# Kernel tuning notes

Hardware: AMD Instinct MI355X
Metric: run time of the kernel (lower is better)

The kernel has to match this reference:

```python
import jax, jax.numpy as jnp
import numpy as np

EMBED_DIM = 1280
NUM_HEADS = 20
HEAD_DIM = EMBED_DIM // NUM_HEADS


def setup_inputs() -> dict:
    key = jax.random.key(0)
    ks = jax.random.split(key, 9)
    s = 0.02
    return {
        "hidden_states": jax.random.normal(ks[0], (4, 1500, EMBED_DIM), dtype=jnp.float32),
        "q_w": jax.random.normal(ks[1], (EMBED_DIM, EMBED_DIM), dtype=jnp.float32) * s,
        "q_b": jax.random.normal(ks[2], (EMBED_DIM,), dtype=jnp.float32) * s,
        "k_w": jax.random.normal(ks[3], (EMBED_DIM, EMBED_DIM), dtype=jnp.float32) * s,
        "v_w": jax.random.normal(ks[4], (EMBED_DIM, EMBED_DIM), dtype=jnp.float32) * s,
        "v_b": jax.random.normal(ks[5], (EMBED_DIM,), dtype=jnp.float32) * s,
        "o_w": jax.random.normal(ks[6], (EMBED_DIM, EMBED_DIM), dtype=jnp.float32) * s,
        "o_b": jax.random.normal(ks[7], (EMBED_DIM,), dtype=jnp.float32) * s,
    }


def reference(hidden_states, q_w, q_b, k_w, v_w, v_b, o_w, o_b):
    B, T, E = hidden_states.shape
    H, D = NUM_HEADS, HEAD_DIM
    scaling = D ** (-0.5)
    # projections (torch Linear: x @ W^T + b)
    q = (hidden_states @ q_w.T + q_b) * scaling
    k = hidden_states @ k_w.T  # k_proj has bias=False
    v = hidden_states @ v_w.T + v_b
    # [B, H, T, D]
    q = q.reshape(B, T, H, D).transpose(0, 2, 1, 3)
    k = k.reshape(B, T, H, D).transpose(0, 2, 1, 3)
    v = v.reshape(B, T, H, D).transpose(0, 2, 1, 3)
    # NOTE: module divides by sqrt(head_dim) AGAIN inside the kernel (faithful)
    scores = jnp.einsum("bhqd,bhkd->bhqk", q, k) / jnp.sqrt(jnp.asarray(D, q.dtype))
    attn = jax.nn.softmax(scores, axis=-1)
    out = jnp.einsum("bhqk,bhkd->bhqd", attn, v)
    out = out.transpose(0, 2, 1, 3).reshape(B, T, E)
    return out @ o_w.T + o_b
```

## Files before the change

### kernel.cpp

```cpp
#include <hip/hip_runtime.h>

typedef __attribute__((ext_vector_type(4))) float f32x4;
typedef __attribute__((ext_vector_type(8))) __bf16 bf16x8;
typedef __attribute__((ext_vector_type(4))) __bf16 bf16x4;

#define DEV __device__ __forceinline__

DEV f32x4 mfma_bf16(bf16x8 a, bf16x8 b, f32x4 c) {
  return __builtin_amdgcn_mfma_f32_16x16x32_bf16(a, b, c, 0, 0, 0);
}

DEV void glds16(const void* gp, void* lp) {
  __builtin_amdgcn_global_load_lds((const __attribute__((address_space(1))) void*)gp,
                                   (__attribute__((address_space(3))) void*)lp, 16, 0, 0);
}

DEV float fast_exp2(float x) {
#if __has_builtin(__builtin_amdgcn_exp2f)
  return __builtin_amdgcn_exp2f(x);
#else
  float r;
  asm("v_exp_f32 %0, %1" : "=v"(r) : "v"(x));
  return r;
#endif
}

#define SB0() __builtin_amdgcn_sched_barrier(0)

__global__ __launch_bounds__(256) void cvt_bf16(const float* __restrict__ in,
                                                __bf16* __restrict__ out, int n_in) {
  long long i = (long long)blockIdx.x * 256 + threadIdx.x;
  long long e = i * 8;
  bf16x8 o = {};
  if (e < n_in) {
    const f32x4* ip = (const f32x4*)(in + e);
    f32x4 a = ip[0], b = ip[1];
#pragma unroll
    for (int j = 0; j < 4; ++j) { o[j] = (__bf16)a[j]; o[j + 4] = (__bf16)b[j]; }
  }
  *(bf16x8*)(out + e) = o;
}

__global__ __launch_bounds__(256) void cvt_w4(const float* __restrict__ a, const float* __restrict__ b,
                                              const float* __restrict__ c, const float* __restrict__ d,
                                              __bf16* __restrict__ oa, __bf16* __restrict__ ob,
                                              __bf16* __restrict__ oc, __bf16* __restrict__ od) {
  int blk = blockIdx.x;
  int which = blk / 800;
  int bb = blk - which * 800;
  const float* in = which == 0 ? a : which == 1 ? b : which == 2 ? c : d;
  __bf16* out = which == 0 ? oa : which == 1 ? ob : which == 2 ? oc : od;
  long long e = ((long long)bb * 256 + threadIdx.x) * 8;
  const f32x4* ip = (const f32x4*)(in + e);
  f32x4 x = ip[0], y = ip[1];
  bf16x8 o;
#pragma unroll
  for (int j = 0; j < 4; ++j) { o[j] = (__bf16)x[j]; o[j + 4] = (__bf16)y[j]; }
  *(bf16x8*)(out + e) = o;
}

__global__ __launch_bounds__(512, 2) void gemm_qkv(const __bf16* __restrict__ A,
                                                   const __bf16* __restrict__ Bw,
                                                   const float* __restrict__ qbias,
                                                   const float* __restrict__ vbias,
                                                   __bf16* __restrict__ Qo,
                                                   __bf16* __restrict__ Ko,
                                                   __bf16* __restrict__ Vto,
                                                   float sq) {
  __shared__ __align__(16) __bf16 lds[3 * 24576];
  const int tid = threadIdx.x;
  const int lane = tid & 63, wave = tid >> 6;
  const int wrow = wave >> 2, wcol = wave & 3;
  const int r = lane & 15, g = lane >> 4;

  const int orig = blockIdx.x;
  const int xcd = orig & 7, ii = orig >> 3;
  const int m_idx = xcd * 6 + ii % 6;
  const int n_idx = ii / 6;
  const int m0 = m_idx * 128, n0 = n_idx * 256;

  const f32x4 fz = {0.f, 0.f, 0.f, 0.f};
  f32x4 acc[4][4];
#pragma unroll
  for (int mi = 0; mi < 4; ++mi)
#pragma unroll
    for (int ni = 0; ni < 4; ++ni) acc[mi][ni] = fz;

  const __bf16* srcA[2];
  const __bf16* srcB[4];
#pragma unroll
  for (int j = 0; j < 2; ++j) {
    const int slot = j * 512 + tid;
    const int row = slot >> 3, ch = slot & 7;
    srcA[j] = A + (size_t)(m0 + row) * 1280 + (ch ^ (row & 7)) * 8;
  }
#pragma unroll
  for (int j = 0; j < 4; ++j) {
    const int slot = j * 512 + tid;
    const int row = slot >> 3, ch = slot & 7;
    srcB[j] = Bw + (size_t)(n0 + row) * 1280 + (ch ^ (row & 7)) * 8;
  }
  const int wdst = wave * 512;

  auto stage_h0 = [&](int buf, int kt2) {
    const int k0 = kt2 * 64;
    glds16(srcA[0] + k0, &lds[buf * 24576 + wdst]);
    glds16(srcA[1] + k0, &lds[buf * 24576 + 4096 + wdst]);
    glds16(srcB[0] + k0, &lds[buf * 24576 + 8192 + wdst]);
  };
  auto stage_h1 = [&](int buf, int kt2) {
    const int k0 = kt2 * 64;
    glds16(srcB[1] + k0, &lds[buf * 24576 + 12288 + wdst]);
    glds16(srcB[2] + k0, &lds[buf * 24576 + 16384 + wdst]);
    glds16(srcB[3] + k0, &lds[buf * 24576 + 20480 + wdst]);
  };

  stage_h0(0, 0); stage_h1(0, 0);
  stage_h0(1, 1); stage_h1(1, 1);
  asm volatile("s_waitcnt vmcnt(6)" ::: "memory");
  SB0();
  __builtin_amdgcn_s_barrier();
  SB0();

  const int aoff = (wrow * 64 + r) * 64;
  const int boff = 8192 + (wcol * 64 + r) * 64;
  const int c0 = (g ^ (r & 7)) * 8;
  const int c1 = ((4 + g) ^ (r & 7)) * 8;

  int cur = 0;
  for (int kt = 0; kt < 20; ++kt) {
    int nxt2 = cur + 2; if (nxt2 >= 3) nxt2 -= 3;
    const __bf16* Lb = &lds[cur * 24576];
    const bool pf = (kt + 2 < 20);

    bf16x8 af[4], bfr[4];
#pragma unroll
    for (int mi = 0; mi < 4; ++mi) af[mi] = *(const bf16x8*)&Lb[aoff + mi * 1024 + c0];
#pragma unroll
    for (int ni = 0; ni < 4; ++ni) bfr[ni] = *(const bf16x8*)&Lb[boff + ni * 1024 + c0];
    if (pf) stage_h0(nxt2, kt + 2);
    asm volatile("s_waitcnt lgkmcnt(0)" ::: "memory");
    SB0();
    __builtin_amdgcn_s_setprio(1);
#pragma unroll
    for (int mi = 0; mi < 4; ++mi)
#pragma unroll
      for (int ni = 0; ni < 4; ++ni)
        acc[mi][ni] = mfma_bf16(af[mi], bfr[ni], acc[mi][ni]);
    __builtin_amdgcn_s_setprio(0);

    bf16x8 af1[4], bfr1[4];
#pragma unroll
    for (int mi = 0; mi < 4; ++mi) af1[mi] = *(const bf16x8*)&Lb[aoff + mi * 1024 + c1];
#pragma unroll
    for (int ni = 0; ni < 4; ++ni) bfr1[ni] = *(const bf16x8*)&Lb[boff + ni * 1024 + c1];
    if (pf) stage_h1(nxt2, kt + 2);
    asm volatile("s_waitcnt lgkmcnt(0)" ::: "memory");
    SB0();
    __builtin_amdgcn_s_setprio(1);
#pragma unroll
    for (int mi = 0; mi < 4; ++mi)
#pragma unroll
      for (int ni = 0; ni < 4; ++ni)
        acc[mi][ni] = mfma_bf16(af1[mi], bfr1[ni], acc[mi][ni]);
    __builtin_amdgcn_s_setprio(0);

    if (pf) asm volatile("s_waitcnt vmcnt(6)" ::: "memory");
    else    asm volatile("s_waitcnt vmcnt(0)" ::: "memory");
    SB0();
    __builtin_amdgcn_s_barrier();
    SB0();
    cur = cur + 1; if (cur >= 3) cur -= 3;
  }

  const int which = n_idx / 5;
  const int nb = n0 - which * 1280 + wcol * 64;
  const float scale = (which == 0) ? sq : 1.f;

#pragma unroll
  for (int ni = 0; ni < 4; ++ni) {
    const int col = nb + ni * 16 + r;
    const float bv = (which == 0) ? qbias[col] : (which == 2) ? vbias[col] : 0.f;
#pragma unroll
    for (int mi = 0; mi < 4; ++mi) {
      if (which == 2) {
        const int row0 = m0 + wrow * 64 + mi * 16 + g * 4;
        if (row0 < 6000) {
          const int bidx = row0 / 1500;
          const int t = row0 - bidx * 1500;
          union { __bf16 h[4]; unsigned long long u; } pk;
#pragma unroll
          for (int rr = 0; rr < 4; ++rr) pk.h[rr] = (__bf16)(acc[mi][ni][rr] + bv);
          *(unsigned long long*)&Vto[((size_t)(bidx * 1280 + col)) * 1536 + t] = pk.u;
        }
      } else {
        __bf16* dst = (which == 0) ? Qo : Ko;
#pragma unroll
        for (int rr = 0; rr < 4; ++rr) {
          const int row = m0 + wrow * 64 + mi * 16 + g * 4 + rr;
          dst[(size_t)row * 1280 + col] = (__bf16)((acc[mi][ni][rr] + bv) * scale);
        }
      }
    }
  }
}

__global__ __launch_bounds__(256) void gemm_o(const __bf16* __restrict__ A,
                                              const __bf16* __restrict__ Bw,
                                              const float* __restrict__ bias,
                                              float* __restrict__ out) {
  __shared__ __align__(16) __bf16 lds[2 * 8192];
  const int tid = threadIdx.x;
  const int lane = tid & 63, wave = tid >> 6;
  const int orig = blockIdx.x;
  const int xcd = orig & 7, i = orig >> 3;
  const int m_idx = (xcd & 3) * 12 + i % 12;
  const int n_idx = (xcd >> 2) * 5 + i / 12;
  const int m0 = m_idx * 128, n0 = n_idx * 128;
  const int wm = (wave >> 1) * 64, wn = (wave & 1) * 64;
  const int r = lane & 15, g = lane >> 4;

  const f32x4 fz = {0.f, 0.f, 0.f, 0.f};
  f32x4 acc[4][4];
#pragma unroll
  for (int mi = 0; mi < 4; ++mi)
#pragma unroll
    for (int ni = 0; ni < 4; ++ni) acc[mi][ni] = fz;

  const int cg = 8 * ((tid & 3) ^ ((tid >> 3) & 3));
  const __bf16* Abase = A + (size_t)(m0 + (tid >> 2)) * 1280 + cg;
  const __bf16* Bbase = Bw + (size_t)(n0 + (tid >> 2)) * 1280 + cg;
  const int wA = wave * 512;
  const int csw = (g ^ ((lane >> 1) & 3)) * 8;

  auto stage = [&](int buf, int kt2) {
    const int k0 = kt2 * 32;
    __bf16* L = &lds[buf * 8192];
    glds16(Abase + k0, L + wA);
    glds16(Abase + 64 * 1280 + k0, L + wA + 2048);
    glds16(Bbase + k0, L + 4096 + wA);
    glds16(Bbase + 64 * 1280 + k0, L + 6144 + wA);
  };

  stage(0, 0);
  for (int kt = 0; kt < 40; ++kt) {
    const int cur = kt & 1;
    if (kt + 1 < 40) {
      stage(cur ^ 1, kt + 1);
      asm volatile("s_waitcnt vmcnt(4)" ::: "memory");
    } else {
      asm volatile("s_waitcnt vmcnt(0)" ::: "memory");
    }
    SB0();
    __builtin_amdgcn_s_barrier();
    SB0();

    const __bf16* Ab = &lds[cur * 8192];
    const __bf16* Bb = Ab + 4096;
    bf16x8 af[4], bfr[4];
#pragma unroll
    for (int mi = 0; mi < 4; ++mi)
      af[mi] = *(const bf16x8*)&Ab[(wm + mi * 16 + r) * 32 + csw];
#pragma unroll
    for (int ni = 0; ni < 4; ++ni)
      bfr[ni] = *(const bf16x8*)&Bb[(wn + ni * 16 + r) * 32 + csw];
#pragma unroll
    for (int mi = 0; mi < 4; ++mi)
#pragma unroll
      for (int ni = 0; ni < 4; ++ni)
        acc[mi][ni] = mfma_bf16(af[mi], bfr[ni], acc[mi][ni]);

    asm volatile("s_waitcnt lgkmcnt(0)" ::: "memory");
    SB0();
    __builtin_amdgcn_s_barrier();
    SB0();
  }

#pragma unroll
  for (int ni = 0; ni < 4; ++ni) {
    const int col = n0 + wn + ni * 16 + r;
    const float bv = bias[col];
#pragma unroll
    for (int mi = 0; mi < 4; ++mi) {
#pragma unroll
      for (int rr = 0; rr < 4; ++rr) {
        const int row = m0 + wm + mi * 16 + g * 4 + rr;
        if (row < 6000) out[(size_t)row * 1280 + col] = acc[mi][ni][rr] + bv;
      }
    }
  }
}

__global__ __launch_bounds__(256) void flash_attn(const __bf16* __restrict__ Qg,
                                                  const __bf16* __restrict__ Kg,
                                                  const __bf16* __restrict__ Vt,
                                                  __bf16* __restrict__ Og) {
  constexpr int TQ = 1500, NKT = 24;
  __shared__ __align__(16) __bf16 lds[16384];

  const int tid = threadIdx.x;
  const int lane = tid & 63, w = tid >> 6;
  const int r = lane & 15, g = lane >> 4;

  const int orig = blockIdx.x;
  const int work = (orig & 7) * 120 + (orig >> 3);
  const int bh = work / 12, qb = work - bh * 12;
  const int b = bh / 20, h = bh - b * 20;
  const int q0 = qb * 128;
  const size_t base = (size_t)b * (TQ * 1280) + h * 64;
  const __bf16* Vt_bh = Vt + (size_t)(b * 1280 + h * 64) * 1536;

  const int k_src_col = 8 * ((lane & 7) ^ (lane >> 3));
  const int k_row_loc = w * 8 + (lane >> 3);
  const int v_d_loc = 8 * w + (lane >> 3);
  const int v_chunk = 8 * ((lane & 7) ^ (lane >> 3));

  bf16x8 qf[2][2];
#pragma unroll
  for (int qs = 0; qs < 2; ++qs) {
    int t = q0 + w * 32 + qs * 16 + r;
    t = t < TQ ? t : TQ - 1;
    const __bf16* qp = Qg + base + (size_t)t * 1280;
#pragma unroll
    for (int dk = 0; dk < 2; ++dk) qf[qs][dk] = *(const bf16x8*)(qp + dk * 32 + g * 8);
  }

  const f32x4 fz = {0.f, 0.f, 0.f, 0.f};
  f32x4 o_acc[2][4];
#pragma unroll
  for (int qs = 0; qs < 2; ++qs)
#pragma unroll
    for (int ni = 0; ni < 4; ++ni) o_acc[qs][ni] = fz;
  float l_run[2] = {0.f, 0.f};

  auto stage = [&](int buf, int kt2) {
    const int kb = kt2 * 64;
#pragma unroll
    for (int i = 0; i < 2; ++i) {
      int row = kb + i * 32 + k_row_loc;
      row = row < TQ ? row : TQ - 1;
      glds16(Kg + base + (size_t)row * 1280 + k_src_col,
             &lds[buf * 8192 + i * 2048 + w * 512]);
    }
#pragma unroll
    for (int i = 0; i < 2; ++i) {
      glds16(Vt_bh + (size_t)(32 * i + v_d_loc) * 1536 + kb + v_chunk,
             &lds[buf * 8192 + 4096 + i * 2048 + w * 512]);
    }
  };

  stage(0, 0);
  __syncthreads();
  for (int kt = 0; kt < NKT; ++kt) {
    const int cur = kt & 1;
    if (kt + 1 < NKT) stage(cur ^ 1, kt + 1);

    const __bf16* Kb = &lds[cur * 8192];

    f32x4 s[2][4];
#pragma unroll
    for (int qs = 0; qs < 2; ++qs)
#pragma unroll
      for (int nt = 0; nt < 4; ++nt) s[qs][nt] = fz;
#pragma unroll
    for (int dk = 0; dk < 2; ++dk) {
      bf16x8 kf[4];
#pragma unroll
      for (int nt = 0; nt < 4; ++nt) {
        const int row = nt * 16 + r;
        const int sc = (dk * 32 + g * 8) ^ ((r & 7) << 3);
        kf[nt] = *(const bf16x8*)&Kb[row * 64 + sc];
      }
#pragma unroll
      for (int qs = 0; qs < 2; ++qs)
#pragma unroll
        for (int nt = 0; nt < 4; ++nt) s[qs][nt] = mfma_bf16(kf[nt], qf[qs][dk], s[qs][nt]);
    }

    if (kt == NKT - 1) {
#pragma unroll
      for (int nt = 0; nt < 4; ++nt)
#pragma unroll
        for (int rr = 0; rr < 4; ++rr) {
          const int key = kt * 64 + nt * 16 + g * 4 + rr;
          if (key >= TQ) { s[0][nt][rr] = -1.0e30f; s[1][nt][rr] = -1.0e30f; }
        }
    }

#pragma unroll
    for (int qs = 0; qs < 2; ++qs) {
      float ssum = 0.f;
#pragma unroll
      for (int nt = 0; nt < 4; ++nt)
#pragma unroll
        for (int rr = 0; rr < 4; ++rr) {
          const float p = fast_exp2(s[qs][nt][rr]);
          s[qs][nt][rr] = p;
          ssum += p;
        }
      l_run[qs] += ssum;
    }

    const __bf16* Vbuf = &lds[cur * 8192 + 4096];
    const int swz = (r & 7) << 3;
#pragma unroll
    for (int ks = 0; ks < 2; ++ks) {
      bf16x8 pa[2];
#pragma unroll
      for (int qs = 0; qs < 2; ++qs) {
        bf16x8 t;
#pragma unroll
        for (int j = 0; j < 4; ++j) {
          t[j] = (__bf16)s[qs][2 * ks][j];
          t[4 + j] = (__bf16)s[qs][2 * ks + 1][j];
        }
        pa[qs] = t;
      }
      const int o1 = (32 * ks + 4 * g) ^ swz;
      const int o2 = (32 * ks + 16 + 4 * g) ^ swz;
#pragma unroll
      for (int ni = 0; ni < 4; ++ni) {
        const int dbase = (16 * ni + r) * 64;
        union { bf16x4 hh[2]; bf16x8 v; } u;
        u.hh[0] = *(const bf16x4*)&Vbuf[dbase + o1];
        u.hh[1] = *(const bf16x4*)&Vbuf[dbase + o2];
#pragma unroll
        for (int qs = 0; qs < 2; ++qs) o_acc[qs][ni] = mfma_bf16(u.v, pa[qs], o_acc[qs][ni]);
      }
    }

    __syncthreads();
  }

  float inv[2];
#pragma unroll
  for (int qs = 0; qs < 2; ++qs) {
    float l = l_run[qs];
    l += __shfl_xor(l, 16);
    l += __shfl_xor(l, 32);
    inv[qs] = 1.0f / l;
  }

  __bf16* Ob = &lds[w * 2304];
#pragma unroll
  for (int qs = 0; qs < 2; ++qs) {
#pragma unroll
    for (int ni = 0; ni < 4; ++ni)
#pragma unroll
      for (int rr = 0; rr < 4; ++rr)
        Ob[(qs * 16 + r) * 72 + ni * 16 + g * 4 + rr] = (__bf16)(o_acc[qs][ni][rr] * inv[qs]);
  }
  __syncthreads();
  const int qg = q0 + w * 32 + (lane >> 1);
  if (qg < TQ) {
#pragma unroll
    for (int v = 0; v < 4; ++v) {
      const int c = (lane & 1) * 32 + v * 8;
      bf16x8 val = *(const bf16x8*)&lds[w * 2304 + (lane >> 1) * 72 + c];
      *(bf16x8*)&Og[base + (size_t)qg * 1280 + c] = val;
    }
  }
}

extern "C" void kernel_launch(void* const* d_in, const int* in_sizes, int n_in,
                              void* d_out, int out_size, void* d_ws, size_t ws_size,
                              hipStream_t stream) {
  const float* hs = (const float*)d_in[0];
  const float* qw = (const float*)d_in[1];
  const float* qb = (const float*)d_in[2];
  const float* kw = (const float*)d_in[3];
  const float* vw = (const float*)d_in[4];
  const float* vb = (const float*)d_in[5];
  const float* ow = (const float*)d_in[6];
  const float* ob = (const float*)d_in[7];

  const long long MP = 6144LL * 1280;
  const long long WE = 1280LL * 1280;
  __bf16* Xb = (__bf16*)d_ws;
  __bf16* Wq = Xb + MP;
  __bf16* Wk = Wq + WE;
  __bf16* Wv = Wk + WE;
  __bf16* Wo = Wv + WE;
  __bf16* Qb = Wo + WE;
  __bf16* Kb = Qb + MP;
  __bf16* Vtb = Kb + MP;
  __bf16* Ab = Xb;

  cvt_bf16<<<3840, 256, 0, stream>>>(hs, Xb, 7680000);
  cvt_w4<<<3200, 256, 0, stream>>>(qw, kw, vw, ow, Wq, Wk, Wv, Wo);

  const float SQ = 1.4426950408889634f / 64.f;
  gemm_qkv<<<720, 512, 0, stream>>>(Xb, Wq, qb, vb, Qb, Kb, Vtb, SQ);

  flash_attn<<<960, 256, 0, stream>>>(Qb, Kb, Vtb, Ab);

  gemm_o<<<480, 256, 0, stream>>>(Ab, Wo, ob, (float*)d_out);
}
```

Baseline: 180.2 us.

## Merge conversion kernels, retile output GEMM with triple buffering, tighten attention sync

Fuses the activation and weight fp32-to-bf16 conversion kernels into one launch to save a launch. Rewrites the output projection GEMM to use 512-thread blocks with 128x256 tiles, K-step 64, a three-stage LDS pipeline with split prefetch and s_setprio around the MFMA blocks. Replaces the __syncthreads in flash attention with explicit vmcnt/lgkmcnt waits plus raw barriers, so the next tile's prefetch is waited on before its use. The larger GEMM tiles leave only 240 blocks, which may underfill the device's compute units.

```diff
diff --git a/kernel.cpp b/kernel.cpp
--- a/kernel.cpp
+++ b/kernel.cpp
@@ -27,36 +27,41 @@
 
 #define SB0() __builtin_amdgcn_sched_barrier(0)
 
-__global__ __launch_bounds__(256) void cvt_bf16(const float* __restrict__ in,
-                                                __bf16* __restrict__ out, int n_in) {
-  long long i = (long long)blockIdx.x * 256 + threadIdx.x;
-  long long e = i * 8;
-  bf16x8 o = {};
-  if (e < n_in) {
+__global__ __launch_bounds__(256) void cvt_all(const float* __restrict__ hs,
+                                               const float* __restrict__ qw,
+                                               const float* __restrict__ kw,
+                                               const float* __restrict__ vw,
+                                               const float* __restrict__ ow,
+                                               __bf16* __restrict__ oX,
+                                               __bf16* __restrict__ oQ,
+                                               __bf16* __restrict__ oK,
+                                               __bf16* __restrict__ oV,
+                                               __bf16* __restrict__ oO) {
+  const int blk = blockIdx.x;
+  if (blk < 3840) {
+    long long e = ((long long)blk * 256 + threadIdx.x) * 8;
+    bf16x8 o = {};
+    if (e < 7680000) {
+      const f32x4* ip = (const f32x4*)(hs + e);
+      f32x4 a = ip[0], b = ip[1];
+#pragma unroll
+      for (int j = 0; j < 4; ++j) { o[j] = (__bf16)a[j]; o[j + 4] = (__bf16)b[j]; }
+    }
+    *(bf16x8*)(oX + e) = o;
+  } else {
+    const int wb = blk - 3840;
+    const int which = wb / 800;
+    const int bb = wb - which * 800;
+    const float* in = which == 0 ? qw : which == 1 ? kw : which == 2 ? vw : ow;
+    __bf16* out = which == 0 ? oQ : which == 1 ? oK : which == 2 ? oV : oO;
+    long long e = ((long long)bb * 256 + threadIdx.x) * 8;
     const f32x4* ip = (const f32x4*)(in + e);
-    f32x4 a = ip[0], b = ip[1];
-#pragma unroll
-    for (int j = 0; j < 4; ++j) { o[j] = (__bf16)a[j]; o[j + 4] = (__bf16)b[j]; }
-  }
-  *(bf16x8*)(out + e) = o;
-}
-
-__global__ __launch_bounds__(256) void cvt_w4(const float* __restrict__ a, const float* __restrict__ b,
-                                              const float* __restrict__ c, const float* __restrict__ d,
-                                              __bf16* __restrict__ oa, __bf16* __restrict__ ob,
-                                              __bf16* __restrict__ oc, __bf16* __restrict__ od) {
-  int blk = blockIdx.x;
-  int which = blk / 800;
-  int bb = blk - which * 800;
-  const float* in = which == 0 ? a : which == 1 ? b : which == 2 ? c : d;
-  __bf16* out = which == 0 ? oa : which == 1 ? ob : which == 2 ? oc : od;
-  long long e = ((long long)bb * 256 + threadIdx.x) * 8;
-  const f32x4* ip = (const f32x4*)(in + e);
-  f32x4 x = ip[0], y = ip[1];
-  bf16x8 o;
-#pragma unroll
-  for (int j = 0; j < 4; ++j) { o[j] = (__bf16)x[j]; o[j + 4] = (__bf16)y[j]; }
-  *(bf16x8*)(out + e) = o;
+    f32x4 x = ip[0], y = ip[1];
+    bf16x8 o;
+#pragma unroll
+    for (int j = 0; j < 4; ++j) { o[j] = (__bf16)x[j]; o[j + 4] = (__bf16)y[j]; }
+    *(bf16x8*)(out + e) = o;
+  }
 }
 
 __global__ __launch_bounds__(512, 2) void gemm_qkv(const __bf16* __restrict__ A,
@@ -205,20 +210,21 @@
   }
 }
 
-__global__ __launch_bounds__(256) void gemm_o(const __bf16* __restrict__ A,
-                                              const __bf16* __restrict__ Bw,
-                                              const float* __restrict__ bias,
-                                              float* __restrict__ out) {
-  __shared__ __align__(16) __bf16 lds[2 * 8192];
+__global__ __launch_bounds__(512, 2) void gemm_o(const __bf16* __restrict__ A,
+                                                 const __bf16* __restrict__ Bw,
+                                                 const float* __restrict__ bias,
+                                                 float* __restrict__ out) {
+  __shared__ __align__(16) __bf16 lds[3 * 24576];
   const int tid = threadIdx.x;
   const int lane = tid & 63, wave = tid >> 6;
+  const int wrow = wave >> 2, wcol = wave & 3;
+  const int r = lane & 15, g = lane >> 4;
+
   const int orig = blockIdx.x;
-  const int xcd = orig & 7, i = orig >> 3;
-  const int m_idx = (xcd & 3) * 12 + i % 12;
-  const int n_idx = (xcd >> 2) * 5 + i / 12;
-  const int m0 = m_idx * 128, n0 = n_idx * 128;
-  const int wm = (wave >> 1) * 64, wn = (wave & 1) * 64;
-  const int r = lane & 15, g = lane >> 4;
+  const int xcd = orig & 7, ii = orig >> 3;
+  const int m_idx = xcd * 6 + ii % 6;
+  const int n_idx = ii / 6;
+  const int m0 = m_idx * 128, n0 = n_idx * 256;
 
   const f32x4 fz = {0.f, 0.f, 0.f, 0.f};
   f32x4 acc[4][4];
@@ -227,64 +233,102 @@
 #pragma unroll
     for (int ni = 0; ni < 4; ++ni) acc[mi][ni] = fz;
 
-  const int cg = 8 * ((tid & 3) ^ ((tid >> 3) & 3));
-  const __bf16* Abase = A + (size_t)(m0 + (tid >> 2)) * 1280 + cg;
-  const __bf16* Bbase = Bw + (size_t)(n0 + (tid >> 2)) * 1280 + cg;
-  const int wA = wave * 512;
-  const int csw = (g ^ ((lane >> 1) & 3)) * 8;
-
-  auto stage = [&](int buf, int kt2) {
-    const int k0 = kt2 * 32;
-    __bf16* L = &lds[buf * 8192];
-    glds16(Abase + k0, L + wA);
-    glds16(Abase + 64 * 1280 + k0, L + wA + 2048);
-    glds16(Bbase + k0, L + 4096 + wA);
-    glds16(Bbase + 64 * 1280 + k0, L + 6144 + wA);
+  const __bf16* srcA[2];
+  const __bf16* srcB[4];
+#pragma unroll
+  for (int j = 0; j < 2; ++j) {
+    const int slot = j * 512 + tid;
+    const int row = slot >> 3, ch = slot & 7;
+    srcA[j] = A + (size_t)(m0 + row) * 1280 + (ch ^ (row & 7)) * 8;
+  }
+#pragma unroll
+  for (int j = 0; j < 4; ++j) {
+    const int slot = j * 512 + tid;
+    const int row = slot >> 3, ch = slot & 7;
+    srcB[j] = Bw + (size_t)(n0 + row) * 1280 + (ch ^ (row & 7)) * 8;
+  }
+  const int wdst = wave * 512;
+
+  auto stage_h0 = [&](int buf, int kt2) {
+    const int k0 = kt2 * 64;
+    glds16(srcA[0] + k0, &lds[buf * 24576 + wdst]);
+    glds16(srcA[1] + k0, &lds[buf * 24576 + 4096 + wdst]);
+    glds16(srcB[0] + k0, &lds[buf * 24576 + 8192 + wdst]);
   };
-
-  stage(0, 0);
-  for (int kt = 0; kt < 40; ++kt) {
-    const int cur = kt & 1;
-    if (kt + 1 < 40) {
-      stage(cur ^ 1, kt + 1);
-      asm volatile("s_waitcnt vmcnt(4)" ::: "memory");
-    } else {
-      asm volatile("s_waitcnt vmcnt(0)" ::: "memory");
-    }
-    SB0();
-    __builtin_amdgcn_s_barrier();
-    SB0();
-
-    const __bf16* Ab = &lds[cur * 8192];
-    const __bf16* Bb = Ab + 4096;
+  auto stage_h1 = [&](int buf, int kt2) {
+    const int k0 = kt2 * 64;
+    glds16(srcB[1] + k0, &lds[buf * 24576 + 12288 + wdst]);
+    glds16(srcB[2] + k0, &lds[buf * 24576 + 16384 + wdst]);
+    glds16(srcB[3] + k0, &lds[buf * 24576 + 20480 + wdst]);
+  };
+
+  stage_h0(0, 0); stage_h1(0, 0);
+  stage_h0(1, 1); stage_h1(1, 1);
+  asm volatile("s_waitcnt vmcnt(6)" ::: "memory");
+  SB0();
+  __builtin_amdgcn_s_barrier();
+  SB0();
+
+  const int aoff = (wrow * 64 + r) * 64;
+  const int boff = 8192 + (wcol * 64 + r) * 64;
+  const int c0 = (g ^ (r & 7)) * 8;
+  const int c1 = ((4 + g) ^ (r & 7)) * 8;
+
+  int cur = 0;
+  for (int kt = 0; kt < 20; ++kt) {
+    int nxt2 = cur + 2; if (nxt2 >= 3) nxt2 -= 3;
+    const __bf16* Lb = &lds[cur * 24576];
+    const bool pf = (kt + 2 < 20);
+
     bf16x8 af[4], bfr[4];
 #pragma unroll
-    for (int mi = 0; mi < 4; ++mi)
-      af[mi] = *(const bf16x8*)&Ab[(wm + mi * 16 + r) * 32 + csw];
-#pragma unroll
-    for (int ni = 0; ni < 4; ++ni)
-      bfr[ni] = *(const bf16x8*)&Bb[(wn + ni * 16 + r) * 32 + csw];
+    for (int mi = 0; mi < 4; ++mi) af[mi] = *(const bf16x8*)&Lb[aoff + mi * 1024 + c0];
+#pragma unroll
+    for (int ni = 0; ni < 4; ++ni) bfr[ni] = *(const bf16x8*)&Lb[boff + ni * 1024 + c0];
+    if (pf) stage_h0(nxt2, kt + 2);
+    asm volatile("s_waitcnt lgkmcnt(0)" ::: "memory");
+    SB0();
+    __builtin_amdgcn_s_setprio(1);
 #pragma unroll
     for (int mi = 0; mi < 4; ++mi)
 #pragma unroll
       for (int ni = 0; ni < 4; ++ni)
         acc[mi][ni] = mfma_bf16(af[mi], bfr[ni], acc[mi][ni]);
-
+    __builtin_amdgcn_s_setprio(0);
+
+    bf16x8 af1[4], bfr1[4];
+#pragma unroll
+    for (int mi = 0; mi < 4; ++mi) af1[mi] = *(const bf16x8*)&Lb[aoff + mi * 1024 + c1];
+#pragma unroll
+    for (int ni = 0; ni < 4; ++ni) bfr1[ni] = *(const bf16x8*)&Lb[boff + ni * 1024 + c1];
+    if (pf) stage_h1(nxt2, kt + 2);
     asm volatile("s_waitcnt lgkmcnt(0)" ::: "memory");
     SB0();
+    __builtin_amdgcn_s_setprio(1);
+#pragma unroll
+    for (int mi = 0; mi < 4; ++mi)
+#pragma unroll
+      for (int ni = 0; ni < 4; ++ni)
+        acc[mi][ni] = mfma_bf16(af1[mi], bfr1[ni], acc[mi][ni]);
+    __builtin_amdgcn_s_setprio(0);
+
+    if (pf) asm volatile("s_waitcnt vmcnt(6)" ::: "memory");
+    else    asm volatile("s_waitcnt vmcnt(0)" ::: "memory");
+    SB0();
     __builtin_amdgcn_s_barrier();
     SB0();
+    cur = cur + 1; if (cur >= 3) cur -= 3;
   }
 
 #pragma unroll
   for (int ni = 0; ni < 4; ++ni) {
-    const int col = n0 + wn + ni * 16 + r;
+    const int col = n0 + wcol * 64 + ni * 16 + r;
     const float bv = bias[col];
 #pragma unroll
     for (int mi = 0; mi < 4; ++mi) {
 #pragma unroll
       for (int rr = 0; rr < 4; ++rr) {
-        const int row = m0 + wm + mi * 16 + g * 4 + rr;
+        const int row = m0 + wrow * 64 + mi * 16 + g * 4 + rr;
         if (row < 6000) out[(size_t)row * 1280 + col] = acc[mi][ni][rr] + bv;
       }
     }
@@ -350,10 +394,17 @@
   };
 
   stage(0, 0);
-  __syncthreads();
   for (int kt = 0; kt < NKT; ++kt) {
     const int cur = kt & 1;
-    if (kt + 1 < NKT) stage(cur ^ 1, kt + 1);
+    if (kt + 1 < NKT) {
+      stage(cur ^ 1, kt + 1);
+      asm volatile("s_waitcnt vmcnt(4)" ::: "memory");
+    } else {
+      asm volatile("s_waitcnt vmcnt(0)" ::: "memory");
+    }
+    SB0();
+    __builtin_amdgcn_s_barrier();
+    SB0();
 
     const __bf16* Kb = &lds[cur * 8192];
 
@@ -429,7 +480,10 @@
       }
     }
 
-    __syncthreads();
+    asm volatile("s_waitcnt lgkmcnt(0)" ::: "memory");
+    SB0();
+    __builtin_amdgcn_s_barrier();
+    SB0();
   }
 
   float inv[2];
@@ -486,13 +540,12 @@
   __bf16* Vtb = Kb + MP;
   __bf16* Ab = Xb;
 
-  cvt_bf16<<<3840, 256, 0, stream>>>(hs, Xb, 7680000);
-  cvt_w4<<<3200, 256, 0, stream>>>(qw, kw, vw, ow, Wq, Wk, Wv, Wo);
+  cvt_all<<<7040, 256, 0, stream>>>(hs, qw, kw, vw, ow, Xb, Wq, Wk, Wv, Wo);
 
   const float SQ = 1.4426950408889634f / 64.f;
   gemm_qkv<<<720, 512, 0, stream>>>(Xb, Wq, qb, vb, Qb, Kb, Vtb, SQ);
 
   flash_attn<<<960, 256, 0, stream>>>(Qb, Kb, Vtb, Ab);
 
-  gemm_o<<<480, 256, 0, stream>>>(Ab, Wo, ob, (float*)d_out);
-}
+  gemm_o<<<240, 512, 0, stream>>>(Ab, Wo, ob, (float*)d_out);
+}
```

New measurement: 175.7 us. -2.5%, faster.
